# Kernel tuning notes

Measured on AMD Instinct MI355X. Metric: run time of the kernel, lower is better.

The kernel has to match this reference:

```python
import jax, jax.numpy as jnp
import numpy as np

TOP_K = 2  # matches init kwarg top_k


def setup_inputs() -> dict:
    key = jax.random.key(0)
    k1, k2, k3 = jax.random.split(key, 3)
    N, D, H, E = 8192, 2048, 2048, 8
    x = jax.random.normal(k1, (N, D), dtype=jnp.float32)
    Wg = jax.random.normal(k2, (D, E), dtype=jnp.float32) * (1.0 / np.sqrt(D))
    bg = jnp.zeros((E,), dtype=jnp.float32)
    We = jax.random.normal(k3, (E, D, H), dtype=jnp.float32) * (1.0 / np.sqrt(D))
    be = jnp.zeros((E, H), dtype=jnp.float32)
    return {"x": x, "Wg": Wg, "bg": bg, "We": We, "be": be}


def reference(x, Wg, bg, We, be):
    # Gating: softmax over experts, then keep only top-k weights per token.
    gate = jax.nn.softmax(x @ Wg + bg, axis=-1)          # [N, E]
    top_v, top_i = jax.lax.top_k(gate, TOP_K)            # [N, K]
    E = gate.shape[-1]
    # Sparse combine weights: zeros except top-k entries (weights NOT renormalized,
    # matching the original which uses raw softmax scores).
    comb = jnp.sum(jax.nn.one_hot(top_i, E, dtype=gate.dtype) * top_v[..., None], axis=1)  # [N, E]
    # Per-expert linear applied to every token (dense dispatch), then weighted sum.
    expert_out = jnp.einsum('nd,edh->neh', x, We) + be   # [N, E, H]
    out = jnp.einsum('ne,neh->nh', comb, expert_out)     # [N, H]
    return out
```

## Files before the change

### kernel.cpp

```cpp
#include <hip/hip_runtime.h>

#define N_TOK 8192
#define DIM   2048
#define HID   2048
#define NE    8
#define NKT   (DIM / 64)

typedef unsigned short u16;
typedef __attribute__((ext_vector_type(4))) float f4v;
typedef __attribute__((ext_vector_type(8))) short s8v;
typedef __attribute__((ext_vector_type(4))) unsigned short us4;

__device__ __forceinline__ unsigned int cvtpk(float lo, float hi) {
  unsigned int r;
  asm volatile("v_cvt_pk_bf16_f32 %0, %1, %2" : "=v"(r) : "v"(lo), "v"(hi));
  return r;
}

__global__ __launch_bounds__(256) void gating_kernel(
    const float* __restrict__ x, const float* __restrict__ Wg,
    const float* __restrict__ bg, int* __restrict__ sel,
    float* __restrict__ wslot)
{
  __shared__ float wg_lds[NE][DIM];
  #pragma unroll
  for (int i = 0; i < 16; ++i) {
    int f = threadIdx.x + 256 * i;
    int d = f >> 1, ep = (f & 1) * 4;
    float4 w = reinterpret_cast<const float4*>(Wg)[f];
    wg_lds[ep + 0][d] = w.x; wg_lds[ep + 1][d] = w.y;
    wg_lds[ep + 2][d] = w.z; wg_lds[ep + 3][d] = w.w;
  }
  __syncthreads();

  int wave = threadIdx.x >> 6, lane = threadIdx.x & 63;
  #pragma unroll 2
  for (int j = 0; j < 4; ++j) {
    int n = blockIdx.x * 16 + wave * 4 + j;
    const float4* x4 = reinterpret_cast<const float4*>(x + (size_t)n * DIM);
    float acc[NE] = {0.f,0.f,0.f,0.f,0.f,0.f,0.f,0.f};
    #pragma unroll
    for (int i = 0; i < 8; ++i) {
      int d4 = lane + 64 * i;
      float4 xv = x4[d4];
      #pragma unroll
      for (int e = 0; e < NE; ++e) {
        float4 w = *reinterpret_cast<const float4*>(&wg_lds[e][d4 * 4]);
        acc[e] += xv.x * w.x + xv.y * w.y + xv.z * w.z + xv.w * w.w;
      }
    }
    #pragma unroll
    for (int e = 0; e < NE; ++e)
      #pragma unroll
      for (int off = 32; off; off >>= 1)
        acc[e] += __shfl_xor(acc[e], off);

    if (lane == 0) {
      float m = -1e30f;
      #pragma unroll
      for (int e = 0; e < NE; ++e) { acc[e] += bg[e]; m = fmaxf(m, acc[e]); }
      float p[NE]; float s = 0.f;
      #pragma unroll
      for (int e = 0; e < NE; ++e) { p[e] = expf(acc[e] - m); s += p[e]; }
      float inv = 1.0f / s;
      int e1 = 0; float v1 = p[0];
      #pragma unroll
      for (int e = 1; e < NE; ++e) if (p[e] > v1) { v1 = p[e]; e1 = e; }
      int e2 = -1; float v2 = -1.f;
      #pragma unroll
      for (int e = 0; e < NE; ++e) if (e != e1 && p[e] > v2) { v2 = p[e]; e2 = e; }
      sel[n] = e1 | (e2 << 4);
      wslot[n] = v1 * inv;
      wslot[N_TOK + n] = v2 * inv;
    }
  }
}

__global__ __launch_bounds__(256) void build_lists_kernel(
    const int* __restrict__ sel, int* __restrict__ counts, int* __restrict__ lists)
{
  __shared__ int wsum[4];
  __shared__ int runbase;
  int b = blockIdx.x;
  int s = b >> 3, e = b & 7;
  int t = threadIdx.x, lane = t & 63, wave = t >> 6;
  if (t == 0) runbase = 0;
  __syncthreads();
  int* listp = lists + (size_t)b * N_TOK;
  for (int base = 0; base < N_TOK; base += 256) {
    int n = base + t;
    int sv = sel[n];
    int field = s ? (sv >> 4) : (sv & 15);
    bool p = (field == e);
    unsigned long long mask = __ballot(p);
    int rank = __popcll(mask & ((1ull << lane) - 1ull));
    int wtot = __popcll(mask);
    if (lane == 0) wsum[wave] = wtot;
    __syncthreads();
    int wbase = 0;
    #pragma unroll
    for (int w = 0; w < 4; ++w) wbase += (w < wave) ? wsum[w] : 0;
    int tot = wsum[0] + wsum[1] + wsum[2] + wsum[3];
    if (p) listp[runbase + wbase + rank] = n;
    __syncthreads();
    if (t == 0) runbase += tot;
    __syncthreads();
  }
  if (t == 0) counts[b] = runbase;
}

__global__ void build_desc_kernel(const int* __restrict__ counts,
                                  int* __restrict__ gfirst, int* __restrict__ desc)
{
  if (threadIdx.x == 0 && blockIdx.x == 0) {
    for (int s = 0; s < 2; ++s) {
      int tc = 0;
      for (int e = 0; e < NE; ++e) {
        gfirst[s * 9 + e] = tc;
        int nt = (counts[s * NE + e] + 127) >> 7;
        for (int i = 0; i < nt; ++i) desc[s * 71 + tc++] = (e << 8) | i;
      }
      gfirst[s * 9 + 8] = tc;
    }
  }
}

template <int PHASE>
__global__ __launch_bounds__(1024, 6) void moe_gemm_f32(
    const float* __restrict__ xf, const float* __restrict__ Wef,
    const float* __restrict__ be, const int* __restrict__ counts,
    const int* __restrict__ gfirst, const int* __restrict__ desc,
    const int* __restrict__ lists, const float* __restrict__ wslot,
    float* __restrict__ out)
{
  __shared__ __align__(16) u16 A_lds[128 * 64];
  __shared__ __align__(16) u16 B_lds[128 * 64];
  __shared__ int   tok_lds[128];
  __shared__ float wgt_lds[128];

  const int ntile = blockIdx.x;
  const int idx   = blockIdx.y;
  if (idx >= gfirst[PHASE * 9 + 8]) return;
  const int d  = desc[PHASE * 71 + idx];
  const int e  = d >> 8;
  const int mt = d & 255;
  const int cnt = counts[PHASE * NE + e];

  const int t = threadIdx.x;
  if (t < 128) {
    int r = mt * 128 + t;
    int rc = (r < cnt) ? r : (cnt - 1);
    int tok = lists[(PHASE * NE + e) * N_TOK + rc];
    tok_lds[t] = tok;
    wgt_lds[t] = wslot[PHASE * N_TOK + tok];
  }
  __syncthreads();

  const int lane = t & 63, wid = t >> 6;
  const int wm = (wid & 3) * 32, wn = (wid >> 2) * 32;

  f4v acc[2][2];
  f4v zero = {0.f, 0.f, 0.f, 0.f};
  #pragma unroll
  for (int mi = 0; mi < 2; ++mi)
    #pragma unroll
    for (int ni = 0; ni < 2; ++ni) acc[mi][ni] = zero;

  const float* wef = Wef + (size_t)e * DIM * HID;

  const float* ap[2]; unsigned int ab[2];
  #pragma unroll
  for (int i = 0; i < 2; ++i) {
    int flat = t + 1024 * i;
    int row = flat >> 4, c4 = flat & 15;
    ap[i] = xf + (size_t)tok_lds[row] * DIM + c4 * 4;
    ab[i] = ((unsigned int)(row * 128 + c4 * 8)) ^ (((unsigned int)row & 7u) << 4);
  }
  const int bn = t & 127, bh = t >> 7;
  const float* bp0 = wef + (size_t)(bh * 8) * HID + ntile * 128 + bn;
  const unsigned int bbyte = ((unsigned int)(bn * 128 + bh * 16)) ^ (((unsigned int)bn & 7u) << 4);

  const int lrow = lane & 15, lkg = lane >> 4;

  #pragma unroll 1
  for (int kt = 0; kt < NKT; ++kt) {
    #pragma unroll
    for (int i = 0; i < 2; ++i) {
      float4 v = *reinterpret_cast<const float4*>(ap[i] + kt * 64);
      uint2 w; w.x = cvtpk(v.x, v.y); w.y = cvtpk(v.z, v.w);
      *reinterpret_cast<uint2*>(reinterpret_cast<char*>(A_lds) + ab[i]) = w;
    }
    {
      const float* bpk = bp0 + (size_t)kt * 64 * HID;
      float bv[8];
      #pragma unroll
      for (int j = 0; j < 8; ++j) bv[j] = bpk[(size_t)j * HID];
      union { unsigned int w[4]; s8v v; } ub;
      ub.w[0] = cvtpk(bv[0], bv[1]); ub.w[1] = cvtpk(bv[2], bv[3]);
      ub.w[2] = cvtpk(bv[4], bv[5]); ub.w[3] = cvtpk(bv[6], bv[7]);
      *reinterpret_cast<s8v*>(reinterpret_cast<char*>(B_lds) + bbyte) = ub.v;
    }
    __syncthreads();
    #pragma unroll
    for (int kk2 = 0; kk2 < 2; ++kk2) {
      s8v a[2], b[2];
      unsigned int koff = (unsigned int)(kk2 * 64 + lkg * 16);
      #pragma unroll
      for (int i = 0; i < 2; ++i) {
        unsigned int arow = (unsigned int)(wm + i * 16 + lrow);
        a[i] = *reinterpret_cast<const s8v*>(
            reinterpret_cast<const char*>(A_lds) + ((arow * 128u + koff) ^ ((arow & 7u) << 4)));
        unsigned int brow = (unsigned int)(wn + i * 16 + lrow);
        b[i] = *reinterpret_cast<const s8v*>(
            reinterpret_cast<const char*>(B_lds) + ((brow * 128u + koff) ^ ((brow & 7u) << 4)));
      }
      #pragma unroll
      for (int mi = 0; mi < 2; ++mi)
        #pragma unroll
        for (int ni = 0; ni < 2; ++ni)
          acc[mi][ni] = __builtin_amdgcn_mfma_f32_16x16x32_bf16(a[mi], b[ni], acc[mi][ni], 0, 0, 0);
    }
    __syncthreads();
  }

  const float* bev = be + (size_t)e * HID + ntile * 128;
  #pragma unroll
  for (int ni = 0; ni < 2; ++ni) {
    int col = wn + ni * 16 + (lane & 15);
    float bevv = bev[col];
    #pragma unroll
    for (int mi = 0; mi < 2; ++mi) {
      #pragma unroll
      for (int q = 0; q < 4; ++q) {
        int row = wm + mi * 16 + (lane >> 4) * 4 + q;
        if (mt * 128 + row < cnt) {
          int tok = tok_lds[row];
          float w = wgt_lds[row];
          float v = w * (acc[mi][ni][q] + bevv);
          float* o = out + (size_t)tok * HID + ntile * 128 + col;
          if (PHASE == 0) *o = v; else *o += v;
        }
      }
    }
  }
}

extern "C" void kernel_launch(void* const* d_in, const int* in_sizes, int n_in,
                              void* d_out, int out_size, void* d_ws, size_t ws_size,
                              hipStream_t stream) {
  const float* x  = (const float*)d_in[0];
  const float* Wg = (const float*)d_in[1];
  const float* bg = (const float*)d_in[2];
  const float* We = (const float*)d_in[3];
  const float* be = (const float*)d_in[4];
  float* out = (float*)d_out;
  char* ws = (char*)d_ws;

  int*   counts = (int*)ws;
  int*   gfirst = (int*)(ws + 64);
  int*   desc   = (int*)(ws + 256);
  int*   sel    = (int*)(ws + 1024);
  float* wslot  = (float*)(ws + 33792);
  int*   lists  = (int*)(ws + 99328);

  hipLaunchKernelGGL(gating_kernel, dim3(512), dim3(256), 0, stream,
                     x, Wg, bg, sel, wslot);
  hipLaunchKernelGGL(build_lists_kernel, dim3(16), dim3(256), 0, stream,
                     sel, counts, lists);
  hipLaunchKernelGGL(build_desc_kernel, dim3(1), dim3(64), 0, stream,
                     counts, gfirst, desc);

  dim3 ggrid(16, 71);
  hipLaunchKernelGGL((moe_gemm_f32<0>), ggrid, dim3(1024), 0, stream,
                     x, We, be, counts, gfirst, desc, lists, wslot, out);
  hipLaunchKernelGGL((moe_gemm_f32<1>), ggrid, dim3(1024), 0, stream,
                     x, We, be, counts, gfirst, desc, lists, wslot, out);
}
```

Measured before the change: 449.9 us.

## Software-pipeline global loads two k-tiles ahead in MoE GEMM

Restructures the k-loop to prefetch global fp32 A and B data into two register sets, issued two tiles ahead, so the loads overlap the MFMA work of the current tile. The launch-bounds occupancy hint is lowered from 6 to 4 to make room for the extra registers. This trades occupancy for latency hiding inside each workgroup and keeps the single LDS buffer with two barriers per tile.

```diff
diff --git a/kernel.cpp b/kernel.cpp
--- a/kernel.cpp
+++ b/kernel.cpp
@@ -9,7 +9,6 @@
 typedef unsigned short u16;
 typedef __attribute__((ext_vector_type(4))) float f4v;
 typedef __attribute__((ext_vector_type(8))) short s8v;
-typedef __attribute__((ext_vector_type(4))) unsigned short us4;
 
 __device__ __forceinline__ unsigned int cvtpk(float lo, float hi) {
   unsigned int r;
@@ -126,7 +125,7 @@
 }
 
 template <int PHASE>
-__global__ __launch_bounds__(1024, 6) void moe_gemm_f32(
+__global__ __launch_bounds__(1024, 4) void moe_gemm_f32(
     const float* __restrict__ xf, const float* __restrict__ Wef,
     const float* __restrict__ be, const int* __restrict__ counts,
     const int* __restrict__ gfirst, const int* __restrict__ desc,
@@ -182,46 +181,71 @@
 
   const int lrow = lane & 15, lkg = lane >> 4;
 
+  float4 sa0_0, sa0_1; float sb0[8];
+  float4 sa1_0, sa1_1; float sb1[8];
+
+#define ISSUE0(KT) do {                                                         \
+    sa0_0 = *reinterpret_cast<const float4*>(ap[0] + (KT) * 64);                \
+    sa0_1 = *reinterpret_cast<const float4*>(ap[1] + (KT) * 64);                \
+    const float* bpk = bp0 + (size_t)(KT) * 64 * HID;                           \
+    _Pragma("unroll") for (int j = 0; j < 8; ++j) sb0[j] = bpk[(size_t)j * HID];\
+  } while (0)
+#define ISSUE1(KT) do {                                                         \
+    sa1_0 = *reinterpret_cast<const float4*>(ap[0] + (KT) * 64);                \
+    sa1_1 = *reinterpret_cast<const float4*>(ap[1] + (KT) * 64);                \
+    const float* bpk = bp0 + (size_t)(KT) * 64 * HID;                           \
+    _Pragma("unroll") for (int j = 0; j < 8; ++j) sb1[j] = bpk[(size_t)j * HID];\
+  } while (0)
+#define WRITE_SET(A0, A1, B) do {                                               \
+    uint2 w0; w0.x = cvtpk(A0.x, A0.y); w0.y = cvtpk(A0.z, A0.w);               \
+    *reinterpret_cast<uint2*>(reinterpret_cast<char*>(A_lds) + ab[0]) = w0;     \
+    uint2 w1; w1.x = cvtpk(A1.x, A1.y); w1.y = cvtpk(A1.z, A1.w);               \
+    *reinterpret_cast<uint2*>(reinterpret_cast<char*>(A_lds) + ab[1]) = w1;     \
+    union { unsigned int w[4]; s8v v; } ub;                                     \
+    ub.w[0] = cvtpk(B[0], B[1]); ub.w[1] = cvtpk(B[2], B[3]);                   \
+    ub.w[2] = cvtpk(B[4], B[5]); ub.w[3] = cvtpk(B[6], B[7]);                   \
+    *reinterpret_cast<s8v*>(reinterpret_cast<char*>(B_lds) + bbyte) = ub.v;     \
+  } while (0)
+#define MMA_STEP() do {                                                         \
+    _Pragma("unroll") for (int kk2 = 0; kk2 < 2; ++kk2) {                       \
+      s8v a[2], b[2];                                                           \
+      unsigned int koff = (unsigned int)(kk2 * 64 + lkg * 16);                  \
+      _Pragma("unroll") for (int i = 0; i < 2; ++i) {                           \
+        unsigned int arow = (unsigned int)(wm + i * 16 + lrow);                 \
+        a[i] = *reinterpret_cast<const s8v*>(reinterpret_cast<const char*>(A_lds)\
+               + ((arow * 128u + koff) ^ ((arow & 7u) << 4)));                  \
+        unsigned int brow = (unsigned int)(wn + i * 16 + lrow);                 \
+        b[i] = *reinterpret_cast<const s8v*>(reinterpret_cast<const char*>(B_lds)\
+               + ((brow * 128u + koff) ^ ((brow & 7u) << 4)));                  \
+      }                                                                         \
+      _Pragma("unroll") for (int mi = 0; mi < 2; ++mi)                          \
+        _Pragma("unroll") for (int ni = 0; ni < 2; ++ni)                        \
+          acc[mi][ni] = __builtin_amdgcn_mfma_f32_16x16x32_bf16(                \
+              a[mi], b[ni], acc[mi][ni], 0, 0, 0);                              \
+    }                                                                           \
+  } while (0)
+
+  ISSUE0(0);
+  ISSUE1(1);
+
   #pragma unroll 1
-  for (int kt = 0; kt < NKT; ++kt) {
-    #pragma unroll
-    for (int i = 0; i < 2; ++i) {
-      float4 v = *reinterpret_cast<const float4*>(ap[i] + kt * 64);
-      uint2 w; w.x = cvtpk(v.x, v.y); w.y = cvtpk(v.z, v.w);
-      *reinterpret_cast<uint2*>(reinterpret_cast<char*>(A_lds) + ab[i]) = w;
-    }
-    {
-      const float* bpk = bp0 + (size_t)kt * 64 * HID;
-      float bv[8];
-      #pragma unroll
-      for (int j = 0; j < 8; ++j) bv[j] = bpk[(size_t)j * HID];
-      union { unsigned int w[4]; s8v v; } ub;
-      ub.w[0] = cvtpk(bv[0], bv[1]); ub.w[1] = cvtpk(bv[2], bv[3]);
-      ub.w[2] = cvtpk(bv[4], bv[5]); ub.w[3] = cvtpk(bv[6], bv[7]);
-      *reinterpret_cast<s8v*>(reinterpret_cast<char*>(B_lds) + bbyte) = ub.v;
-    }
-    __syncthreads();
-    #pragma unroll
-    for (int kk2 = 0; kk2 < 2; ++kk2) {
-      s8v a[2], b[2];
-      unsigned int koff = (unsigned int)(kk2 * 64 + lkg * 16);
-      #pragma unroll
-      for (int i = 0; i < 2; ++i) {
-        unsigned int arow = (unsigned int)(wm + i * 16 + lrow);
-        a[i] = *reinterpret_cast<const s8v*>(
-            reinterpret_cast<const char*>(A_lds) + ((arow * 128u + koff) ^ ((arow & 7u) << 4)));
-        unsigned int brow = (unsigned int)(wn + i * 16 + lrow);
-        b[i] = *reinterpret_cast<const s8v*>(
-            reinterpret_cast<const char*>(B_lds) + ((brow * 128u + koff) ^ ((brow & 7u) << 4)));
-      }
-      #pragma unroll
-      for (int mi = 0; mi < 2; ++mi)
-        #pragma unroll
-        for (int ni = 0; ni < 2; ++ni)
-          acc[mi][ni] = __builtin_amdgcn_mfma_f32_16x16x32_bf16(a[mi], b[ni], acc[mi][ni], 0, 0, 0);
-    }
-    __syncthreads();
-  }
+  for (int kt = 0; kt < NKT; kt += 2) {
+    WRITE_SET(sa0_0, sa0_1, sb0);
+    __syncthreads();
+    if (kt + 2 < NKT) ISSUE0(kt + 2);
+    MMA_STEP();
+    __syncthreads();
+    WRITE_SET(sa1_0, sa1_1, sb1);
+    __syncthreads();
+    if (kt + 3 < NKT) ISSUE1(kt + 3);
+    MMA_STEP();
+    __syncthreads();
+  }
+
+#undef ISSUE0
+#undef ISSUE1
+#undef WRITE_SET
+#undef MMA_STEP
 
   const float* bev = be + (size_t)e * HID + ntile * 128;
   #pragma unroll
```

Result: no change. 456.0 us (+1.3%).

## Double K-tile to 128 and halve block to 512 threads with wider warp tiles

Applied to the files above, without the earlier changes.

The MoE GEMM's K-tile grows from 64 to 128, which halves the number of K iterations and the barrier pairs per tile. The block shrinks to 512 threads, so each wave now computes a 32x64 output (2x4 MFMA tiles), raising MFMA work per LDS fragment load. All global loads for a K-step are issued before the conversions and LDS stores, and the LDS swizzle is widened to 16 units to match the 256-byte rows. This adds registers (32 B floats, 8 float4s, 8 accumulators) and doubles LDS use, which may reduce occupancy.

```diff
diff --git a/kernel.cpp b/kernel.cpp
--- a/kernel.cpp
+++ b/kernel.cpp
@@ -4,12 +4,12 @@
 #define DIM   2048
 #define HID   2048
 #define NE    8
-#define NKT   (DIM / 64)
+#define BK    128
+#define NKT   (DIM / BK)
 
 typedef unsigned short u16;
 typedef __attribute__((ext_vector_type(4))) float f4v;
 typedef __attribute__((ext_vector_type(8))) short s8v;
-typedef __attribute__((ext_vector_type(4))) unsigned short us4;
 
 __device__ __forceinline__ unsigned int cvtpk(float lo, float hi) {
   unsigned int r;
@@ -126,15 +126,15 @@
 }
 
 template <int PHASE>
-__global__ __launch_bounds__(1024, 6) void moe_gemm_f32(
+__global__ __launch_bounds__(512) void moe_gemm_f32(
     const float* __restrict__ xf, const float* __restrict__ Wef,
     const float* __restrict__ be, const int* __restrict__ counts,
     const int* __restrict__ gfirst, const int* __restrict__ desc,
     const int* __restrict__ lists, const float* __restrict__ wslot,
     float* __restrict__ out)
 {
-  __shared__ __align__(16) u16 A_lds[128 * 64];
-  __shared__ __align__(16) u16 B_lds[128 * 64];
+  __shared__ __align__(16) u16 A_lds[128 * BK];
+  __shared__ __align__(16) u16 B_lds[128 * BK];
   __shared__ int   tok_lds[128];
   __shared__ float wgt_lds[128];
 
@@ -157,67 +157,83 @@
   __syncthreads();
 
   const int lane = t & 63, wid = t >> 6;
-  const int wm = (wid & 3) * 32, wn = (wid >> 2) * 32;
-
-  f4v acc[2][2];
+  const int wm = (wid & 3) * 32, wn = (wid >> 2) * 64;
+  const int lrow = lane & 15, lkg = lane >> 4;
+
+  f4v acc[2][4];
   f4v zero = {0.f, 0.f, 0.f, 0.f};
   #pragma unroll
   for (int mi = 0; mi < 2; ++mi)
     #pragma unroll
-    for (int ni = 0; ni < 2; ++ni) acc[mi][ni] = zero;
+    for (int ni = 0; ni < 4; ++ni) acc[mi][ni] = zero;
 
   const float* wef = Wef + (size_t)e * DIM * HID;
 
-  const float* ap[2]; unsigned int ab[2];
-  #pragma unroll
-  for (int i = 0; i < 2; ++i) {
-    int flat = t + 1024 * i;
-    int row = flat >> 4, c4 = flat & 15;
+  const float* ap[8]; unsigned int ab[8];
+  #pragma unroll
+  for (int i = 0; i < 8; ++i) {
+    int flat = t + 512 * i;
+    int row = flat >> 5, c4 = flat & 31;
     ap[i] = xf + (size_t)tok_lds[row] * DIM + c4 * 4;
-    ab[i] = ((unsigned int)(row * 128 + c4 * 8)) ^ (((unsigned int)row & 7u) << 4);
+    ab[i] = (unsigned int)(row * 256)
+          + ((((unsigned int)(c4 >> 1) ^ ((unsigned int)row & 15u)) << 4)
+             | (((unsigned int)c4 & 1u) << 3));
   }
   const int bn = t & 127, bh = t >> 7;
-  const float* bp0 = wef + (size_t)(bh * 8) * HID + ntile * 128 + bn;
-  const unsigned int bbyte = ((unsigned int)(bn * 128 + bh * 16)) ^ (((unsigned int)bn & 7u) << 4);
-
-  const int lrow = lane & 15, lkg = lane >> 4;
+  const float* bp0 = wef + (size_t)(bh * 32) * HID + ntile * 128 + bn;
+  unsigned int bbyte[4];
+  #pragma unroll
+  for (int q = 0; q < 4; ++q)
+    bbyte[q] = (unsigned int)(bn * 256)
+             + (((unsigned int)(bh * 4 + q) ^ ((unsigned int)bn & 15u)) << 4);
 
   #pragma unroll 1
   for (int kt = 0; kt < NKT; ++kt) {
-    #pragma unroll
-    for (int i = 0; i < 2; ++i) {
-      float4 v = *reinterpret_cast<const float4*>(ap[i] + kt * 64);
-      uint2 w; w.x = cvtpk(v.x, v.y); w.y = cvtpk(v.z, v.w);
+    float4 av[8];
+    #pragma unroll
+    for (int i = 0; i < 8; ++i)
+      av[i] = *reinterpret_cast<const float4*>(ap[i] + kt * BK);
+    float bv[32];
+    const float* bpk = bp0 + (size_t)kt * BK * HID;
+    #pragma unroll
+    for (int j = 0; j < 32; ++j)
+      bv[j] = bpk[(size_t)j * HID];
+
+    #pragma unroll
+    for (int i = 0; i < 8; ++i) {
+      uint2 w; w.x = cvtpk(av[i].x, av[i].y); w.y = cvtpk(av[i].z, av[i].w);
       *reinterpret_cast<uint2*>(reinterpret_cast<char*>(A_lds) + ab[i]) = w;
     }
-    {
-      const float* bpk = bp0 + (size_t)kt * 64 * HID;
-      float bv[8];
-      #pragma unroll
-      for (int j = 0; j < 8; ++j) bv[j] = bpk[(size_t)j * HID];
+    #pragma unroll
+    for (int q = 0; q < 4; ++q) {
       union { unsigned int w[4]; s8v v; } ub;
-      ub.w[0] = cvtpk(bv[0], bv[1]); ub.w[1] = cvtpk(bv[2], bv[3]);
-      ub.w[2] = cvtpk(bv[4], bv[5]); ub.w[3] = cvtpk(bv[6], bv[7]);
-      *reinterpret_cast<s8v*>(reinterpret_cast<char*>(B_lds) + bbyte) = ub.v;
-    }
-    __syncthreads();
-    #pragma unroll
-    for (int kk2 = 0; kk2 < 2; ++kk2) {
-      s8v a[2], b[2];
-      unsigned int koff = (unsigned int)(kk2 * 64 + lkg * 16);
+      ub.w[0] = cvtpk(bv[q * 8 + 0], bv[q * 8 + 1]);
+      ub.w[1] = cvtpk(bv[q * 8 + 2], bv[q * 8 + 3]);
+      ub.w[2] = cvtpk(bv[q * 8 + 4], bv[q * 8 + 5]);
+      ub.w[3] = cvtpk(bv[q * 8 + 6], bv[q * 8 + 7]);
+      *reinterpret_cast<s8v*>(reinterpret_cast<char*>(B_lds) + bbyte[q]) = ub.v;
+    }
+    __syncthreads();
+    #pragma unroll
+    for (int kk = 0; kk < 4; ++kk) {
+      unsigned int unit = (unsigned int)(kk * 4 + lkg);
+      s8v a[2], b[4];
       #pragma unroll
       for (int i = 0; i < 2; ++i) {
         unsigned int arow = (unsigned int)(wm + i * 16 + lrow);
-        a[i] = *reinterpret_cast<const s8v*>(
-            reinterpret_cast<const char*>(A_lds) + ((arow * 128u + koff) ^ ((arow & 7u) << 4)));
+        a[i] = *reinterpret_cast<const s8v*>(reinterpret_cast<const char*>(A_lds)
+               + arow * 256u + ((unit ^ (arow & 15u)) << 4));
+      }
+      #pragma unroll
+      for (int i = 0; i < 4; ++i) {
         unsigned int brow = (unsigned int)(wn + i * 16 + lrow);
-        b[i] = *reinterpret_cast<const s8v*>(
-            reinterpret_cast<const char*>(B_lds) + ((brow * 128u + koff) ^ ((brow & 7u) << 4)));
+        b[i] = *reinterpret_cast<const s8v*>(reinterpret_cast<const char*>(B_lds)
+               + brow * 256u + ((unit ^ (brow & 15u)) << 4));
       }
       #pragma unroll
       for (int mi = 0; mi < 2; ++mi)
         #pragma unroll
-        for (int ni = 0; ni < 2; ++ni)
+        for (int ni = 0; ni < 4; ++ni)
           acc[mi][ni] = __builtin_amdgcn_mfma_f32_16x16x32_bf16(a[mi], b[ni], acc[mi][ni], 0, 0, 0);
     }
     __syncthreads();
@@ -225,14 +241,14 @@
 
   const float* bev = be + (size_t)e * HID + ntile * 128;
   #pragma unroll
-  for (int ni = 0; ni < 2; ++ni) {
-    int col = wn + ni * 16 + (lane & 15);
+  for (int ni = 0; ni < 4; ++ni) {
+    int col = wn + ni * 16 + lrow;
     float bevv = bev[col];
     #pragma unroll
     for (int mi = 0; mi < 2; ++mi) {
       #pragma unroll
       for (int q = 0; q < 4; ++q) {
-        int row = wm + mi * 16 + (lane >> 4) * 4 + q;
+        int row = wm + mi * 16 + lkg * 4 + q;
         if (mt * 128 + row < cnt) {
           int tok = tok_lds[row];
           float w = wgt_lds[row];
@@ -271,8 +287,8 @@
                      counts, gfirst, desc);
 
   dim3 ggrid(16, 71);
-  hipLaunchKernelGGL((moe_gemm_f32<0>), ggrid, dim3(1024), 0, stream,
+  hipLaunchKernelGGL((moe_gemm_f32<0>), ggrid, dim3(512), 0, stream,
                      x, We, be, counts, gfirst, desc, lists, wslot, out);
-  hipLaunchKernelGGL((moe_gemm_f32<1>), ggrid, dim3(1024), 0, stream,
+  hipLaunchKernelGGL((moe_gemm_f32<1>), ggrid, dim3(512), 0, stream,
                      x, We, be, counts, gfirst, desc, lists, wslot, out);
 }
```

Measured after the change: 531.9 us. +18.2%, slower.

## Warp-specialize MoE GEMM into producer and consumer waves with double-buffered LDS

Applied to the files above, without the earlier changes.

Shrinks the GEMM block from 1024 to 512 threads and splits it into 4 producer waves and 4 consumer waves. Producers load fp32 x and We tiles two k-steps ahead in registers, convert them to bf16 and write into double-buffered LDS. Consumers each compute a 64x64 sub-tile with 4x4 MFMA accumulators. The aim is to overlap global loads with MFMA work and give each wave more work per LDS fragment. The cost is higher register pressure (64 floats of B and 64 floats of A prefetch per producer thread) and lower occupancy. The pipeline depends on raw s_barrier pairing, where producers exit early and consumers issue one barrier per k-step.

```diff
diff --git a/kernel.cpp b/kernel.cpp
--- a/kernel.cpp
+++ b/kernel.cpp
@@ -4,18 +4,20 @@
 #define DIM   2048
 #define HID   2048
 #define NE    8
-#define NKT   (DIM / 64)
+#define BK    64
+#define NKT   (DIM / BK)
 
 typedef unsigned short u16;
 typedef __attribute__((ext_vector_type(4))) float f4v;
 typedef __attribute__((ext_vector_type(8))) short s8v;
-typedef __attribute__((ext_vector_type(4))) unsigned short us4;
 
 __device__ __forceinline__ unsigned int cvtpk(float lo, float hi) {
   unsigned int r;
   asm volatile("v_cvt_pk_bf16_f32 %0, %1, %2" : "=v"(r) : "v"(lo), "v"(hi));
   return r;
 }
+#define BAR()  asm volatile("s_barrier" ::: "memory")
+#define LGKM0() asm volatile("s_waitcnt lgkmcnt(0)" ::: "memory")
 
 __global__ __launch_bounds__(256) void gating_kernel(
     const float* __restrict__ x, const float* __restrict__ Wg,
@@ -126,15 +128,15 @@
 }
 
 template <int PHASE>
-__global__ __launch_bounds__(1024, 6) void moe_gemm_f32(
+__global__ __launch_bounds__(512) void moe_gemm_f32(
     const float* __restrict__ xf, const float* __restrict__ Wef,
     const float* __restrict__ be, const int* __restrict__ counts,
     const int* __restrict__ gfirst, const int* __restrict__ desc,
     const int* __restrict__ lists, const float* __restrict__ wslot,
     float* __restrict__ out)
 {
-  __shared__ __align__(16) u16 A_lds[128 * 64];
-  __shared__ __align__(16) u16 B_lds[128 * 64];
+  __shared__ __align__(16) u16 A_lds[2][128 * 64];
+  __shared__ __align__(16) u16 B_lds[2][128 * 64];
   __shared__ int   tok_lds[128];
   __shared__ float wgt_lds[128];
 
@@ -157,82 +159,118 @@
   __syncthreads();
 
   const int lane = t & 63, wid = t >> 6;
-  const int wm = (wid & 3) * 32, wn = (wid >> 2) * 32;
-
-  f4v acc[2][2];
+  const float* wef = Wef + (size_t)e * DIM * HID;
+
+  if (wid < 4) {
+    const int p = t;
+    size_t aoff[8]; unsigned int ab[8];
+    #pragma unroll
+    for (int i = 0; i < 8; ++i) {
+      int flat = p + 256 * i;
+      int row = flat >> 4, c4 = flat & 15;
+      aoff[i] = (size_t)tok_lds[row] * DIM + c4 * 4;
+      ab[i] = ((unsigned int)(row * 128 + c4 * 8)) ^ (((unsigned int)row & 7u) << 4);
+    }
+    const int bn = p & 127, bh = p >> 7;
+    const float* bp0 = wef + (size_t)(bh * 32) * HID + ntile * 128 + bn;
+    unsigned int bbyte[8];
+    #pragma unroll
+    for (int kb = 0; kb < 8; ++kb)
+      bbyte[kb] = ((unsigned int)(bn * 128 + bh * 64 + kb * 8)) ^ (((unsigned int)bn & 7u) << 4);
+
+    float4 av0[8], av1[8];
+    float  bv0[32], bv1[32];
+
+#define P_ISSUE(AV, BV, KT) do {                                                  \
+    _Pragma("unroll") for (int i = 0; i < 8; ++i)                                 \
+      AV[i] = *reinterpret_cast<const float4*>(xf + aoff[i] + (KT) * 64);         \
+    const float* bpk = bp0 + (size_t)(KT) * 64 * HID;                             \
+    _Pragma("unroll") for (int j = 0; j < 32; ++j)                                \
+      BV[j] = bpk[(size_t)j * HID];                                               \
+  } while (0)
+#define P_WRITE(AV, BV, BUF) do {                                                 \
+    char* abase = reinterpret_cast<char*>(&A_lds[BUF][0]);                        \
+    char* bbase = reinterpret_cast<char*>(&B_lds[BUF][0]);                        \
+    _Pragma("unroll") for (int i = 0; i < 8; ++i) {                               \
+      uint2 w; w.x = cvtpk(AV[i].x, AV[i].y); w.y = cvtpk(AV[i].z, AV[i].w);      \
+      *reinterpret_cast<uint2*>(abase + ab[i]) = w;                               \
+    }                                                                             \
+    _Pragma("unroll") for (int kb = 0; kb < 8; ++kb) {                            \
+      uint2 w; w.x = cvtpk(BV[kb*4+0], BV[kb*4+1]);                               \
+               w.y = cvtpk(BV[kb*4+2], BV[kb*4+3]);                               \
+      *reinterpret_cast<uint2*>(bbase + bbyte[kb]) = w;                           \
+    }                                                                             \
+  } while (0)
+
+    P_ISSUE(av0, bv0, 0);
+    P_ISSUE(av1, bv1, 1);
+    P_WRITE(av0, bv0, 0);
+    LGKM0();
+
+    #pragma unroll 1
+    for (int kt = 0; kt < NKT; ++kt) {
+      BAR();
+      if (kt & 1) {
+        if (kt + 1 < NKT) P_WRITE(av0, bv0, 0);
+        if (kt + 2 < NKT) P_ISSUE(av1, bv1, kt + 2);
+      } else {
+        if (kt + 1 < NKT) P_WRITE(av1, bv1, 1);
+        if (kt + 2 < NKT) P_ISSUE(av0, bv0, kt + 2);
+      }
+      LGKM0();
+    }
+#undef P_ISSUE
+#undef P_WRITE
+    return;
+  }
+
+  const int cw = wid - 4;
+  const int wm = (cw & 1) * 64, wn = (cw >> 1) * 64;
+  const int lrow = lane & 15, lkg = lane >> 4;
+
+  f4v acc[4][4];
   f4v zero = {0.f, 0.f, 0.f, 0.f};
   #pragma unroll
-  for (int mi = 0; mi < 2; ++mi)
-    #pragma unroll
-    for (int ni = 0; ni < 2; ++ni) acc[mi][ni] = zero;
-
-  const float* wef = Wef + (size_t)e * DIM * HID;
-
-  const float* ap[2]; unsigned int ab[2];
-  #pragma unroll
-  for (int i = 0; i < 2; ++i) {
-    int flat = t + 1024 * i;
-    int row = flat >> 4, c4 = flat & 15;
-    ap[i] = xf + (size_t)tok_lds[row] * DIM + c4 * 4;
-    ab[i] = ((unsigned int)(row * 128 + c4 * 8)) ^ (((unsigned int)row & 7u) << 4);
-  }
-  const int bn = t & 127, bh = t >> 7;
-  const float* bp0 = wef + (size_t)(bh * 8) * HID + ntile * 128 + bn;
-  const unsigned int bbyte = ((unsigned int)(bn * 128 + bh * 16)) ^ (((unsigned int)bn & 7u) << 4);
-
-  const int lrow = lane & 15, lkg = lane >> 4;
+  for (int mi = 0; mi < 4; ++mi)
+    #pragma unroll
+    for (int ni = 0; ni < 4; ++ni) acc[mi][ni] = zero;
 
   #pragma unroll 1
   for (int kt = 0; kt < NKT; ++kt) {
-    #pragma unroll
-    for (int i = 0; i < 2; ++i) {
-      float4 v = *reinterpret_cast<const float4*>(ap[i] + kt * 64);
-      uint2 w; w.x = cvtpk(v.x, v.y); w.y = cvtpk(v.z, v.w);
-      *reinterpret_cast<uint2*>(reinterpret_cast<char*>(A_lds) + ab[i]) = w;
-    }
-    {
-      const float* bpk = bp0 + (size_t)kt * 64 * HID;
-      float bv[8];
-      #pragma unroll
-      for (int j = 0; j < 8; ++j) bv[j] = bpk[(size_t)j * HID];
-      union { unsigned int w[4]; s8v v; } ub;
-      ub.w[0] = cvtpk(bv[0], bv[1]); ub.w[1] = cvtpk(bv[2], bv[3]);
-      ub.w[2] = cvtpk(bv[4], bv[5]); ub.w[3] = cvtpk(bv[6], bv[7]);
-      *reinterpret_cast<s8v*>(reinterpret_cast<char*>(B_lds) + bbyte) = ub.v;
-    }
-    __syncthreads();
+    BAR();
+    const u16* Ab = &A_lds[kt & 1][0];
+    const u16* Bb = &B_lds[kt & 1][0];
     #pragma unroll
     for (int kk2 = 0; kk2 < 2; ++kk2) {
-      s8v a[2], b[2];
+      s8v a[4], b[4];
       unsigned int koff = (unsigned int)(kk2 * 64 + lkg * 16);
       #pragma unroll
-      for (int i = 0; i < 2; ++i) {
+      for (int i = 0; i < 4; ++i) {
         unsigned int arow = (unsigned int)(wm + i * 16 + lrow);
         a[i] = *reinterpret_cast<const s8v*>(
-            reinterpret_cast<const char*>(A_lds) + ((arow * 128u + koff) ^ ((arow & 7u) << 4)));
+            reinterpret_cast<const char*>(Ab) + ((arow * 128u + koff) ^ ((arow & 7u) << 4)));
         unsigned int brow = (unsigned int)(wn + i * 16 + lrow);
         b[i] = *reinterpret_cast<const s8v*>(
-            reinterpret_cast<const char*>(B_lds) + ((brow * 128u + koff) ^ ((brow & 7u) << 4)));
-      }
-      #pragma unroll
-      for (int mi = 0; mi < 2; ++mi)
+            reinterpret_cast<const char*>(Bb) + ((brow * 128u + koff) ^ ((brow & 7u) << 4)));
+      }
+      #pragma unroll
+      for (int mi = 0; mi < 4; ++mi)
         #pragma unroll
-        for (int ni = 0; ni < 2; ++ni)
+        for (int ni = 0; ni < 4; ++ni)
           acc[mi][ni] = __builtin_amdgcn_mfma_f32_16x16x32_bf16(a[mi], b[ni], acc[mi][ni], 0, 0, 0);
     }
-    __syncthreads();
   }
 
   const float* bev = be + (size_t)e * HID + ntile * 128;
   #pragma unroll
-  for (int ni = 0; ni < 2; ++ni) {
-    int col = wn + ni * 16 + (lane & 15);
+  for (int ni = 0; ni < 4; ++ni) {
+    int col = wn + ni * 16 + lrow;
     float bevv = bev[col];
     #pragma unroll
-    for (int mi = 0; mi < 2; ++mi) {
+    for (int mi = 0; mi < 4; ++mi) {
       #pragma unroll
       for (int q = 0; q < 4; ++q) {
-        int row = wm + mi * 16 + (lane >> 4) * 4 + q;
+        int row = wm + mi * 16 + lkg * 4 + q;
         if (mt * 128 + row < cnt) {
           int tok = tok_lds[row];
           float w = wgt_lds[row];
@@ -271,8 +309,8 @@
                      counts, gfirst, desc);
 
   dim3 ggrid(16, 71);
-  hipLaunchKernelGGL((moe_gemm_f32<0>), ggrid, dim3(1024), 0, stream,
+  hipLaunchKernelGGL((moe_gemm_f32<0>), ggrid, dim3(512), 0, stream,
                      x, We, be, counts, gfirst, desc, lists, wslot, out);
-  hipLaunchKernelGGL((moe_gemm_f32<1>), ggrid, dim3(1024), 0, stream,
+  hipLaunchKernelGGL((moe_gemm_f32<1>), ggrid, dim3(512), 0, stream,
                      x, We, be, counts, gfirst, desc, lists, wslot, out);
 }
```

New measurement: 640.1 us. 42.3% more time.
